# Kernel tuning notes

Hardware: AMD Instinct MI355X
Metric: run time of the kernel (lower is better)

The kernel has to match this reference:

```python
import jax, jax.numpy as jnp
import numpy as np

B, S, T, V, D = 256, 256, 256, 512, 512


def _gru_cell(x, h, Wih, Whh, bih, bhh):
    # torch GRU semantics: gates ordered [r, z, n]
    gi = x @ Wih.T + bih            # [B, 3D]
    gh = h @ Whh.T + bhh            # [B, 3D]
    gi_r, gi_z, gi_n = jnp.split(gi, 3, axis=-1)
    gh_r, gh_z, gh_n = jnp.split(gh, 3, axis=-1)
    r = jax.nn.sigmoid(gi_r + gh_r)
    z = jax.nn.sigmoid(gi_z + gh_z)
    n = jnp.tanh(gi_n + r * gh_n)
    return (1.0 - z) * n + z * h


def setup_inputs() -> dict:
    key = jax.random.key(0)
    ks = jax.random.split(key, 14)
    s = 0.05
    inp = {
        "src": jax.random.randint(ks[0], (B, S), 0, V),
        "trg": jax.random.randint(ks[1], (B, T), 0, V),
        "src_mask": jnp.ones((B, S), dtype=bool),
        "trg_mask": jnp.ones((B, T), dtype=bool),
        "enc_emb": jax.random.normal(ks[2], (V, D), jnp.float32) * s,
        "enc_Wih": jax.random.normal(ks[3], (3 * D, D), jnp.float32) * s,
        "enc_Whh": jax.random.normal(ks[4], (3 * D, D), jnp.float32) * s,
        "enc_bih": jnp.zeros((3 * D,), jnp.float32),
        "enc_bhh": jnp.zeros((3 * D,), jnp.float32),
        "dec_emb": jax.random.normal(ks[5], (V, D), jnp.float32) * s,
        "dec_Wih": jax.random.normal(ks[6], (3 * D, D), jnp.float32) * s,
        "dec_Whh": jax.random.normal(ks[7], (3 * D, D), jnp.float32) * s,
        "dec_bih": jnp.zeros((3 * D,), jnp.float32),
        "dec_bhh": jnp.zeros((3 * D,), jnp.float32),
        "out_W": jax.random.normal(ks[8], (V, D), jnp.float32) * s,
        "out_b": jnp.zeros((V,), jnp.float32),
    }
    return inp


def reference(src, trg, src_mask, trg_mask,
              enc_emb, enc_Wih, enc_Whh, enc_bih, enc_bhh,
              dec_emb, dec_Wih, dec_Whh, dec_bih, dec_bhh,
              out_W, out_b):
    b = src.shape[0]
    d = enc_Whh.shape[1]

    # ---- encoder: embed (eval: no dropout) + GRU over src ----
    enc_x = enc_emb[src]                       # [B, S, D]
    h0 = jnp.zeros((b, d), enc_emb.dtype)

    def enc_step(h, x):
        return _gru_cell(x, h, enc_Wih, enc_Whh, enc_bih, enc_bhh), None

    h_enc, _ = jax.lax.scan(enc_step, h0, jnp.swapaxes(enc_x, 0, 1))

    # ---- decoder: relu(embed) + GRU step + linear per timestep ----
    dec_x = jax.nn.relu(dec_emb[trg])          # [B, T, D]

    def dec_step(h, x):
        h = _gru_cell(x, h, dec_Wih, dec_Whh, dec_bih, dec_bhh)
        logits = h @ out_W.T + out_b           # [B, V]
        return h, logits

    _, logits = jax.lax.scan(dec_step, h_enc, jnp.swapaxes(dec_x, 0, 1))
    logits = jnp.swapaxes(logits, 0, 1)        # [B, T, V]
    return jax.nn.log_softmax(logits, axis=-1)
```

## Files before the change

### kernel.cpp

```cpp
#include <hip/hip_runtime.h>
#include <cstdint>
#include <cstddef>

namespace {
constexpr int Dh = 512;
constexpr int G3 = 1536;
constexpr int NB = 256;
constexpr int SL = 256;
constexpr int TL = 256;
constexpr int NV = 512;
}

typedef __attribute__((ext_vector_type(8))) short bf16x8;
typedef __attribute__((ext_vector_type(4))) float f32x4;

__device__ __forceinline__ unsigned short f2bf(float f) {
  unsigned int u = __float_as_uint(f);
  u = (u + 0x7FFFu + ((u >> 16) & 1u)) >> 16;
  return (unsigned short)u;
}
__device__ __forceinline__ float bf2f(unsigned short s) {
  return __uint_as_float(((unsigned int)s) << 16);
}

__global__ __launch_bounds__(256) void cvt_bf16(const float* __restrict__ in,
                                                unsigned short* __restrict__ out,
                                                int n4, int relu) {
  int i = blockIdx.x * 256 + threadIdx.x;
  if (i >= n4) return;
  float4 v = ((const float4*)in)[i];
  if (relu) {
    v.x = fmaxf(v.x, 0.f); v.y = fmaxf(v.y, 0.f);
    v.z = fmaxf(v.z, 0.f); v.w = fmaxf(v.w, 0.f);
  }
  ushort4 o;
  o.x = f2bf(v.x); o.y = f2bf(v.y); o.z = f2bf(v.z); o.w = f2bf(v.w);
  ((ushort4*)out)[i] = o;
}

template <int AMODE, bool OUTBF16>
__global__ __launch_bounds__(256) void gemm_bf16(
    const unsigned short* __restrict__ Abase, const int* __restrict__ idx,
    const unsigned short* __restrict__ W, const float* __restrict__ bias,
    void* __restrict__ Cout, int N) {
  __shared__ unsigned short lds_a[8 * 128 * 8];
  __shared__ unsigned short lds_b[8 * 128 * 8];
  const int t = threadIdx.x;
  const int n0 = blockIdx.x * 128;
  const int m0 = blockIdx.y * 128;
  const int w = t >> 6, l = t & 63;
  const int mq = (w & 1) * 64, nq = (w >> 1) * 64;
  const int l15 = l & 15, lh = l >> 4;

  const int sm = t & 127;
  const int sk = (t >> 7) * 4;
  const unsigned short* arow;
  if (AMODE == 0) {
    arow = Abase + (size_t)idx[m0 + sm] * Dh;
  } else {
    int row = m0 + sm;
    arow = Abase + ((size_t)(row & 255) * NB + (row >> 8)) * Dh;
  }
  const unsigned short* brow = W + (size_t)(n0 + sm) * Dh;

  f32x4 acc[4][4];
#pragma unroll
  for (int i = 0; i < 4; ++i)
#pragma unroll
    for (int j = 0; j < 4; ++j) acc[i][j] = (f32x4)0.f;

  for (int k0 = 0; k0 < Dh; k0 += 64) {
    __syncthreads();
#pragma unroll
    for (int i = 0; i < 4; ++i) {
      int kc = sk + i;
      *(uint4*)&lds_a[(kc * 128 + sm) * 8] = *(const uint4*)(arow + k0 + kc * 8);
      *(uint4*)&lds_b[(kc * 128 + sm) * 8] = *(const uint4*)(brow + k0 + kc * 8);
    }
    __syncthreads();
#pragma unroll
    for (int q = 0; q < 2; ++q) {
      bf16x8 af[4], bfr[4];
#pragma unroll
      for (int i = 0; i < 4; ++i)
        af[i] = *(const bf16x8*)&lds_a[((q * 4 + lh) * 128 + mq + i * 16 + l15) * 8];
#pragma unroll
      for (int j = 0; j < 4; ++j)
        bfr[j] = *(const bf16x8*)&lds_b[((q * 4 + lh) * 128 + nq + j * 16 + l15) * 8];
#pragma unroll
      for (int i = 0; i < 4; ++i)
#pragma unroll
        for (int j = 0; j < 4; ++j)
          acc[i][j] = __builtin_amdgcn_mfma_f32_16x16x32_bf16(af[i], bfr[j], acc[i][j], 0, 0, 0);
    }
  }

#pragma unroll
  for (int j = 0; j < 4; ++j) {
    const int col = n0 + nq + j * 16 + l15;
    const float bv = bias[col];
#pragma unroll
    for (int i = 0; i < 4; ++i) {
#pragma unroll
      for (int r = 0; r < 4; ++r) {
        const size_t row = (size_t)m0 + mq + i * 16 + lh * 4 + r;
        const float v = acc[i][j][r] + bv;
        if (OUTBF16)
          ((unsigned short*)Cout)[row * N + col] = f2bf(v);
        else
          ((float*)Cout)[row * N + col] = v;
      }
    }
  }
}

__global__ __launch_bounds__(256) void gru_step(
    const float* __restrict__ h_in, const unsigned short* __restrict__ hb_in,
    float* __restrict__ h_out, unsigned short* __restrict__ hb_out,
    const unsigned short* __restrict__ W,
    const unsigned short* __restrict__ gi,
    const float* __restrict__ bhh, int tstep, int seq) {
  __shared__ unsigned short lds_w[64 * 48 * 8];
  __shared__ float lds_red[4 * 6 * 256];
  const int t = threadIdx.x;
  const int d0 = blockIdx.x * 16;
  const int b0 = blockIdx.y * 32;
  const int w = t >> 6, l = t & 63;
  const int l15 = l & 15, lh = l >> 4;

#pragma unroll
  for (int i = 0; i < 12; ++i) {
    int id = i * 256 + t;
    int kc = id & 63, c = id >> 6;
    int gate = c >> 4, dl = c & 15;
    const unsigned short* src = W + (size_t)(gate * Dh + d0 + dl) * Dh + kc * 8;
    *(uint4*)&lds_w[(kc * 48 + c) * 8] = *(const uint4*)src;
  }

  f32x4 acc[2][3];
#pragma unroll
  for (int mi = 0; mi < 2; ++mi)
#pragma unroll
    for (int nj = 0; nj < 3; ++nj) acc[mi][nj] = (f32x4)0.f;

  __syncthreads();

#pragma unroll
  for (int q = 0; q < 4; ++q) {
    const int kc32 = w * 4 + q;
    bf16x8 a[2], bfr[3];
#pragma unroll
    for (int mi = 0; mi < 2; ++mi)
      a[mi] = *(const bf16x8*)(hb_in + (size_t)(b0 + mi * 16 + l15) * Dh + kc32 * 32 + lh * 8);
#pragma unroll
    for (int nj = 0; nj < 3; ++nj)
      bfr[nj] = *(const bf16x8*)&lds_w[((kc32 * 4 + lh) * 48 + nj * 16 + l15) * 8];
#pragma unroll
    for (int mi = 0; mi < 2; ++mi)
#pragma unroll
      for (int nj = 0; nj < 3; ++nj)
        acc[mi][nj] = __builtin_amdgcn_mfma_f32_16x16x32_bf16(a[mi], bfr[nj], acc[mi][nj], 0, 0, 0);
  }

#pragma unroll
  for (int mi = 0; mi < 2; ++mi)
#pragma unroll
    for (int nj = 0; nj < 3; ++nj)
#pragma unroll
      for (int r = 0; r < 4; ++r)
        lds_red[(w * 6 + mi * 3 + nj) * 256 + (lh * 4 + r) * 16 + l15] = acc[mi][nj][r];
  __syncthreads();

  const int bl = t >> 3;
  const int dl = (t & 7) * 2;
  const int mi = bl >> 4, row = bl & 15;
  float gh[3][2];
#pragma unroll
  for (int g = 0; g < 3; ++g)
#pragma unroll
    for (int dd = 0; dd < 2; ++dd) {
      float s = 0.f;
#pragma unroll
      for (int ww = 0; ww < 4; ++ww)
        s += lds_red[(ww * 6 + mi * 3 + g) * 256 + row * 16 + dl + dd];
      gh[g][dd] = s;
    }

  const int b = b0 + bl;
  const int d = d0 + dl;
  const unsigned short* gr = gi + ((size_t)b * seq + tstep) * G3;
  ushort2 ur = *(const ushort2*)&gr[d];
  ushort2 uz = *(const ushort2*)&gr[Dh + d];
  ushort2 un = *(const ushort2*)&gr[2 * Dh + d];
  float2 hp = *(const float2*)&h_in[(size_t)b * Dh + d];
  float2 br = *(const float2*)&bhh[d];
  float2 bz = *(const float2*)&bhh[Dh + d];
  float2 bn = *(const float2*)&bhh[2 * Dh + d];
  const float gir[2] = {bf2f(ur.x), bf2f(ur.y)};
  const float giz[2] = {bf2f(uz.x), bf2f(uz.y)};
  const float gin[2] = {bf2f(un.x), bf2f(un.y)};
  const float brv[2] = {br.x, br.y}, bzv[2] = {bz.x, bz.y}, bnv[2] = {bn.x, bn.y};
  const float hpv[2] = {hp.x, hp.y};
  float o[2];
#pragma unroll
  for (int dd = 0; dd < 2; ++dd) {
    float rr = 1.f / (1.f + expf(-(gir[dd] + gh[0][dd] + brv[dd])));
    float zz = 1.f / (1.f + expf(-(giz[dd] + gh[1][dd] + bzv[dd])));
    float nn = tanhf(gin[dd] + rr * (gh[2][dd] + bnv[dd]));
    o[dd] = (1.f - zz) * nn + zz * hpv[dd];
  }
  float2 ov; ov.x = o[0]; ov.y = o[1];
  *(float2*)&h_out[(size_t)b * Dh + d] = ov;
  ushort2 ob; ob.x = f2bf(o[0]); ob.y = f2bf(o[1]);
  *(ushort2*)&hb_out[(size_t)b * Dh + d] = ob;
}

__global__ __launch_bounds__(256) void logsoftmax512(float* __restrict__ x) {
  const int row = blockIdx.x * 4 + (threadIdx.x >> 6);
  const int lane = threadIdx.x & 63;
  float* p = x + (size_t)row * NV + lane * 8;
  float4 v0 = *(const float4*)p;
  float4 v1 = *(const float4*)(p + 4);
  float m = fmaxf(fmaxf(fmaxf(v0.x, v0.y), fmaxf(v0.z, v0.w)),
                  fmaxf(fmaxf(v1.x, v1.y), fmaxf(v1.z, v1.w)));
#pragma unroll
  for (int o = 1; o < 64; o <<= 1) m = fmaxf(m, __shfl_xor(m, o, 64));
  float s = expf(v0.x - m) + expf(v0.y - m) + expf(v0.z - m) + expf(v0.w - m) +
            expf(v1.x - m) + expf(v1.y - m) + expf(v1.z - m) + expf(v1.w - m);
#pragma unroll
  for (int o = 1; o < 64; o <<= 1) s += __shfl_xor(s, o, 64);
  const float ls = m + logf(s);
  v0.x -= ls; v0.y -= ls; v0.z -= ls; v0.w -= ls;
  v1.x -= ls; v1.y -= ls; v1.z -= ls; v1.w -= ls;
  *(float4*)p = v0;
  *(float4*)(p + 4) = v1;
}

extern "C" void kernel_launch(void* const* d_in, const int* in_sizes, int n_in,
                              void* d_out, int out_size, void* d_ws, size_t ws_size,
                              hipStream_t stream) {
  (void)in_sizes; (void)n_in; (void)out_size; (void)ws_size;
  const int* src = (const int*)d_in[0];
  const int* trg = (const int*)d_in[1];
  const float* enc_emb = (const float*)d_in[4];
  const float* enc_Wih = (const float*)d_in[5];
  const float* enc_Whh = (const float*)d_in[6];
  const float* enc_bih = (const float*)d_in[7];
  const float* enc_bhh = (const float*)d_in[8];
  const float* dec_emb = (const float*)d_in[9];
  const float* dec_Wih = (const float*)d_in[10];
  const float* dec_Whh = (const float*)d_in[11];
  const float* dec_bih = (const float*)d_in[12];
  const float* dec_bhh = (const float*)d_in[13];
  const float* out_W = (const float*)d_in[14];
  const float* out_b = (const float*)d_in[15];

  char* ws = (char*)d_ws;
  size_t off = 0;
  auto alloc = [&](size_t bytes) -> char* {
    char* p = ws + off;
    off += (bytes + 255) & ~(size_t)255;
    return p;
  };
  typedef unsigned short u16;
  u16* gi = (u16*)alloc((size_t)NB * SL * G3 * 2);
  u16* hb_all = (u16*)alloc((size_t)TL * NB * Dh * 2);
  float* h_a = (float*)alloc((size_t)NB * Dh * 4);
  float* h_b = (float*)alloc((size_t)NB * Dh * 4);
  u16* hb_a = (u16*)alloc((size_t)NB * Dh * 2);
  u16* hb_b = (u16*)alloc((size_t)NB * Dh * 2);
  u16* embB_e = (u16*)alloc((size_t)NV * Dh * 2);
  u16* embB_d = (u16*)alloc((size_t)NV * Dh * 2);
  u16* WihB_e = (u16*)alloc((size_t)G3 * Dh * 2);
  u16* WhhB_e = (u16*)alloc((size_t)G3 * Dh * 2);
  u16* WihB_d = (u16*)alloc((size_t)G3 * Dh * 2);
  u16* WhhB_d = (u16*)alloc((size_t)G3 * Dh * 2);
  u16* outWB = (u16*)alloc((size_t)NV * Dh * 2);

  cvt_bf16<<<(NV * Dh / 4 + 255) / 256, 256, 0, stream>>>(enc_emb, embB_e, NV * Dh / 4, 0);
  cvt_bf16<<<(NV * Dh / 4 + 255) / 256, 256, 0, stream>>>(dec_emb, embB_d, NV * Dh / 4, 1);
  cvt_bf16<<<(G3 * Dh / 4 + 255) / 256, 256, 0, stream>>>(enc_Wih, WihB_e, G3 * Dh / 4, 0);
  cvt_bf16<<<(G3 * Dh / 4 + 255) / 256, 256, 0, stream>>>(enc_Whh, WhhB_e, G3 * Dh / 4, 0);
  cvt_bf16<<<(G3 * Dh / 4 + 255) / 256, 256, 0, stream>>>(dec_Wih, WihB_d, G3 * Dh / 4, 0);
  cvt_bf16<<<(G3 * Dh / 4 + 255) / 256, 256, 0, stream>>>(dec_Whh, WhhB_d, G3 * Dh / 4, 0);
  cvt_bf16<<<(NV * Dh / 4 + 255) / 256, 256, 0, stream>>>(out_W, outWB, NV * Dh / 4, 0);
  hipMemsetAsync(h_a, 0, (size_t)NB * Dh * 4, stream);
  hipMemsetAsync(hb_a, 0, (size_t)NB * Dh * 2, stream);

  dim3 ggi(G3 / 128, NB * SL / 128);
  gemm_bf16<0, true><<<ggi, 256, 0, stream>>>(embB_e, src, WihB_e, enc_bih, gi, G3);

  dim3 gstep(Dh / 16, NB / 32);
  for (int t = 0; t < SL; ++t) {
    const float* hi = (t & 1) ? h_b : h_a;
    float* ho = (t & 1) ? h_a : h_b;
    const u16* hbi = (t & 1) ? hb_b : hb_a;
    u16* hbo = (t & 1) ? hb_a : hb_b;
    gru_step<<<gstep, 256, 0, stream>>>(hi, hbi, ho, hbo, WhhB_e, gi, enc_bhh, t, SL);
  }

  gemm_bf16<0, true><<<ggi, 256, 0, stream>>>(embB_d, trg, WihB_d, dec_bih, gi, G3);

  for (int t = 0; t < TL; ++t) {
    const float* hi = (t & 1) ? h_b : h_a;
    float* ho = (t & 1) ? h_a : h_b;
    const u16* hbi = (t == 0) ? hb_a : (hb_all + (size_t)(t - 1) * NB * Dh);
    u16* hbo = hb_all + (size_t)t * NB * Dh;
    gru_step<<<gstep, 256, 0, stream>>>(hi, hbi, ho, hbo, WhhB_d, gi, dec_bhh, t, TL);
  }

  dim3 glg(NV / 128, NB * TL / 128);
  gemm_bf16<1, false><<<glg, 256, 0, stream>>>(hb_all, nullptr, outWB, out_b, d_out, NV);
  logsoftmax512<<<NB * TL / 4, 256, 0, stream>>>((float*)d_out);
}
```

Baseline: 3.787 ms.

## Fuse GRU timestep launches into a persistent cooperative kernel with grid barriers

Replaces the 256 per-timestep launches in both the encoder and the decoder with one cooperative persistent kernel per phase. Steps are separated by an atomic-counter grid barrier. The Whh tile fragments stay in registers and the fp32 hidden state stays in registers across steps, so the weight reload from memory and the per-step launch overhead go away. In exchange, each step now pays a global spin barrier. The barrier also depends on cross-block memory visibility through a single-thread release/acquire, which could expose stale cached reads.

```diff
diff --git a/kernel.cpp b/kernel.cpp
--- a/kernel.cpp
+++ b/kernel.cpp
@@ -114,17 +114,23 @@
   }
 }
 
-__global__ __launch_bounds__(256) void gru_step(
-    const float* __restrict__ h_in, const unsigned short* __restrict__ hb_in,
-    float* __restrict__ h_out, unsigned short* __restrict__ hb_out,
+__global__ __launch_bounds__(256) void gru_phase(
     const unsigned short* __restrict__ W,
     const unsigned short* __restrict__ gi,
-    const float* __restrict__ bhh, int tstep, int seq) {
+    const float* __restrict__ bhh,
+    unsigned short* __restrict__ hb0,
+    unsigned short* __restrict__ hb1,
+    const float* __restrict__ h0_in,
+    float* __restrict__ h_final,
+    unsigned short* __restrict__ hb_all,
+    unsigned int* __restrict__ counter,
+    int nsteps) {
   __shared__ unsigned short lds_w[64 * 48 * 8];
   __shared__ float lds_red[4 * 6 * 256];
   const int t = threadIdx.x;
-  const int d0 = blockIdx.x * 16;
-  const int b0 = blockIdx.y * 32;
+  const int bid = blockIdx.x;
+  const int d0 = (bid & 31) * 16;
+  const int b0 = (bid >> 5) * 32;
   const int w = t >> 6, l = t & 63;
   const int l15 = l & 15, lh = l >> 4;
 
@@ -132,87 +138,125 @@
   for (int i = 0; i < 12; ++i) {
     int id = i * 256 + t;
     int kc = id & 63, c = id >> 6;
-    int gate = c >> 4, dl = c & 15;
-    const unsigned short* src = W + (size_t)(gate * Dh + d0 + dl) * Dh + kc * 8;
+    int gate = c >> 4, dl_ = c & 15;
+    const unsigned short* src = W + (size_t)(gate * Dh + d0 + dl_) * Dh + kc * 8;
     *(uint4*)&lds_w[(kc * 48 + c) * 8] = *(const uint4*)src;
   }
-
-  f32x4 acc[2][3];
-#pragma unroll
-  for (int mi = 0; mi < 2; ++mi)
-#pragma unroll
-    for (int nj = 0; nj < 3; ++nj) acc[mi][nj] = (f32x4)0.f;
-
   __syncthreads();
 
+  bf16x8 bfr[4][3];
 #pragma unroll
   for (int q = 0; q < 4; ++q) {
     const int kc32 = w * 4 + q;
-    bf16x8 a[2], bfr[3];
-#pragma unroll
-    for (int mi = 0; mi < 2; ++mi)
-      a[mi] = *(const bf16x8*)(hb_in + (size_t)(b0 + mi * 16 + l15) * Dh + kc32 * 32 + lh * 8);
 #pragma unroll
     for (int nj = 0; nj < 3; ++nj)
-      bfr[nj] = *(const bf16x8*)&lds_w[((kc32 * 4 + lh) * 48 + nj * 16 + l15) * 8];
-#pragma unroll
-    for (int mi = 0; mi < 2; ++mi)
-#pragma unroll
-      for (int nj = 0; nj < 3; ++nj)
-        acc[mi][nj] = __builtin_amdgcn_mfma_f32_16x16x32_bf16(a[mi], bfr[nj], acc[mi][nj], 0, 0, 0);
-  }
-
-#pragma unroll
-  for (int mi = 0; mi < 2; ++mi)
-#pragma unroll
-    for (int nj = 0; nj < 3; ++nj)
-#pragma unroll
-      for (int r = 0; r < 4; ++r)
-        lds_red[(w * 6 + mi * 3 + nj) * 256 + (lh * 4 + r) * 16 + l15] = acc[mi][nj][r];
-  __syncthreads();
+      bfr[q][nj] = *(const bf16x8*)&lds_w[((kc32 * 4 + lh) * 48 + nj * 16 + l15) * 8];
+  }
 
   const int bl = t >> 3;
   const int dl = (t & 7) * 2;
-  const int mi = bl >> 4, row = bl & 15;
-  float gh[3][2];
-#pragma unroll
-  for (int g = 0; g < 3; ++g)
-#pragma unroll
-    for (int dd = 0; dd < 2; ++dd) {
-      float s = 0.f;
-#pragma unroll
-      for (int ww = 0; ww < 4; ++ww)
-        s += lds_red[(ww * 6 + mi * 3 + g) * 256 + row * 16 + dl + dd];
-      gh[g][dd] = s;
-    }
-
+  const int mi_e = bl >> 4, row_e = bl & 15;
   const int b = b0 + bl;
   const int d = d0 + dl;
-  const unsigned short* gr = gi + ((size_t)b * seq + tstep) * G3;
-  ushort2 ur = *(const ushort2*)&gr[d];
-  ushort2 uz = *(const ushort2*)&gr[Dh + d];
-  ushort2 un = *(const ushort2*)&gr[2 * Dh + d];
-  float2 hp = *(const float2*)&h_in[(size_t)b * Dh + d];
-  float2 br = *(const float2*)&bhh[d];
-  float2 bz = *(const float2*)&bhh[Dh + d];
-  float2 bn = *(const float2*)&bhh[2 * Dh + d];
-  const float gir[2] = {bf2f(ur.x), bf2f(ur.y)};
-  const float giz[2] = {bf2f(uz.x), bf2f(uz.y)};
-  const float gin[2] = {bf2f(un.x), bf2f(un.y)};
-  const float brv[2] = {br.x, br.y}, bzv[2] = {bz.x, bz.y}, bnv[2] = {bn.x, bn.y};
-  const float hpv[2] = {hp.x, hp.y};
-  float o[2];
-#pragma unroll
-  for (int dd = 0; dd < 2; ++dd) {
-    float rr = 1.f / (1.f + expf(-(gir[dd] + gh[0][dd] + brv[dd])));
-    float zz = 1.f / (1.f + expf(-(giz[dd] + gh[1][dd] + bzv[dd])));
-    float nn = tanhf(gin[dd] + rr * (gh[2][dd] + bnv[dd]));
-    o[dd] = (1.f - zz) * nn + zz * hpv[dd];
-  }
-  float2 ov; ov.x = o[0]; ov.y = o[1];
-  *(float2*)&h_out[(size_t)b * Dh + d] = ov;
-  ushort2 ob; ob.x = f2bf(o[0]); ob.y = f2bf(o[1]);
-  *(ushort2*)&hb_out[(size_t)b * Dh + d] = ob;
+  const float2 br = *(const float2*)&bhh[d];
+  const float2 bz = *(const float2*)&bhh[Dh + d];
+  const float2 bn = *(const float2*)&bhh[2 * Dh + d];
+  float2 hp;
+  if (h0_in) hp = *(const float2*)&h0_in[(size_t)b * Dh + d];
+  else { hp.x = 0.f; hp.y = 0.f; }
+
+  size_t aoff[2];
+#pragma unroll
+  for (int mi = 0; mi < 2; ++mi)
+    aoff[mi] = (size_t)(b0 + mi * 16 + l15) * Dh + w * 128 + lh * 8;
+
+  const unsigned short* gbase = gi + (size_t)b * 256 * G3;
+  ushort2 ur = *(const ushort2*)&gbase[d];
+  ushort2 uz = *(const ushort2*)&gbase[Dh + d];
+  ushort2 un = *(const ushort2*)&gbase[2 * Dh + d];
+
+  for (int s = 0; s < nsteps; ++s) {
+    const unsigned short* hin = (s & 1) ? hb1 : hb0;
+    unsigned short* hout = (s & 1) ? hb0 : hb1;
+
+    f32x4 acc[2][3];
+#pragma unroll
+    for (int mi = 0; mi < 2; ++mi)
+#pragma unroll
+      for (int nj = 0; nj < 3; ++nj) acc[mi][nj] = (f32x4)0.f;
+
+#pragma unroll
+    for (int q = 0; q < 4; ++q) {
+      bf16x8 a[2];
+#pragma unroll
+      for (int mi = 0; mi < 2; ++mi)
+        a[mi] = *(const bf16x8*)(hin + aoff[mi] + q * 32);
+#pragma unroll
+      for (int mi = 0; mi < 2; ++mi)
+#pragma unroll
+        for (int nj = 0; nj < 3; ++nj)
+          acc[mi][nj] = __builtin_amdgcn_mfma_f32_16x16x32_bf16(a[mi], bfr[q][nj], acc[mi][nj], 0, 0, 0);
+    }
+
+    __syncthreads();
+#pragma unroll
+    for (int mi = 0; mi < 2; ++mi)
+#pragma unroll
+      for (int nj = 0; nj < 3; ++nj)
+#pragma unroll
+        for (int r = 0; r < 4; ++r)
+          lds_red[(w * 6 + mi * 3 + nj) * 256 + (lh * 4 + r) * 16 + l15] = acc[mi][nj][r];
+    __syncthreads();
+
+    float gh[3][2];
+#pragma unroll
+    for (int g = 0; g < 3; ++g)
+#pragma unroll
+      for (int dd = 0; dd < 2; ++dd) {
+        float ssum = 0.f;
+#pragma unroll
+        for (int ww = 0; ww < 4; ++ww)
+          ssum += lds_red[(ww * 6 + mi_e * 3 + g) * 256 + row_e * 16 + dl + dd];
+        gh[g][dd] = ssum;
+      }
+
+    const float gir[2] = {bf2f(ur.x), bf2f(ur.y)};
+    const float giz[2] = {bf2f(uz.x), bf2f(uz.y)};
+    const float gin[2] = {bf2f(un.x), bf2f(un.y)};
+    const float brv[2] = {br.x, br.y}, bzv[2] = {bz.x, bz.y}, bnv[2] = {bn.x, bn.y};
+    float hpv[2] = {hp.x, hp.y};
+    float o[2];
+#pragma unroll
+    for (int dd = 0; dd < 2; ++dd) {
+      float rr = 1.f / (1.f + expf(-(gir[dd] + gh[0][dd] + brv[dd])));
+      float zz = 1.f / (1.f + expf(-(giz[dd] + gh[1][dd] + bzv[dd])));
+      float nn = tanhf(gin[dd] + rr * (gh[2][dd] + bnv[dd]));
+      o[dd] = (1.f - zz) * nn + zz * hpv[dd];
+    }
+    hp.x = o[0]; hp.y = o[1];
+
+    ushort2 ob; ob.x = f2bf(o[0]); ob.y = f2bf(o[1]);
+    *(ushort2*)&hout[(size_t)b * Dh + d] = ob;
+    if (hb_all) *(ushort2*)&hb_all[((size_t)s * NB + b) * Dh + d] = ob;
+    if (h_final && s == nsteps - 1) *(float2*)&h_final[(size_t)b * Dh + d] = hp;
+
+    if (s + 1 < nsteps) {
+      const unsigned short* gr = gbase + (size_t)(s + 1) * G3;
+      ur = *(const ushort2*)&gr[d];
+      uz = *(const ushort2*)&gr[Dh + d];
+      un = *(const ushort2*)&gr[2 * Dh + d];
+    }
+
+    if (s + 1 < nsteps) {
+      __syncthreads();
+      if (t == 0) {
+        __hip_atomic_fetch_add(counter, 1u, __ATOMIC_RELEASE, __HIP_MEMORY_SCOPE_AGENT);
+        const unsigned int tgt = 256u * (unsigned)(s + 1);
+        while (__hip_atomic_load(counter, __ATOMIC_ACQUIRE, __HIP_MEMORY_SCOPE_AGENT) < tgt) {}
+      }
+      __syncthreads();
+    }
+  }
 }
 
 __global__ __launch_bounds__(256) void logsoftmax512(float* __restrict__ x) {
@@ -265,10 +309,9 @@
   typedef unsigned short u16;
   u16* gi = (u16*)alloc((size_t)NB * SL * G3 * 2);
   u16* hb_all = (u16*)alloc((size_t)TL * NB * Dh * 2);
-  float* h_a = (float*)alloc((size_t)NB * Dh * 4);
-  float* h_b = (float*)alloc((size_t)NB * Dh * 4);
-  u16* hb_a = (u16*)alloc((size_t)NB * Dh * 2);
-  u16* hb_b = (u16*)alloc((size_t)NB * Dh * 2);
+  u16* hb0 = (u16*)alloc((size_t)NB * Dh * 2);
+  u16* hb1 = (u16*)alloc((size_t)NB * Dh * 2);
+  float* h_enc = (float*)alloc((size_t)NB * Dh * 4);
   u16* embB_e = (u16*)alloc((size_t)NV * Dh * 2);
   u16* embB_d = (u16*)alloc((size_t)NV * Dh * 2);
   u16* WihB_e = (u16*)alloc((size_t)G3 * Dh * 2);
@@ -276,6 +319,7 @@
   u16* WihB_d = (u16*)alloc((size_t)G3 * Dh * 2);
   u16* WhhB_d = (u16*)alloc((size_t)G3 * Dh * 2);
   u16* outWB = (u16*)alloc((size_t)NV * Dh * 2);
+  unsigned int* ctr = (unsigned int*)alloc(256);
 
   cvt_bf16<<<(NV * Dh / 4 + 255) / 256, 256, 0, stream>>>(enc_emb, embB_e, NV * Dh / 4, 0);
   cvt_bf16<<<(NV * Dh / 4 + 255) / 256, 256, 0, stream>>>(dec_emb, embB_d, NV * Dh / 4, 1);
@@ -284,29 +328,31 @@
   cvt_bf16<<<(G3 * Dh / 4 + 255) / 256, 256, 0, stream>>>(dec_Wih, WihB_d, G3 * Dh / 4, 0);
   cvt_bf16<<<(G3 * Dh / 4 + 255) / 256, 256, 0, stream>>>(dec_Whh, WhhB_d, G3 * Dh / 4, 0);
   cvt_bf16<<<(NV * Dh / 4 + 255) / 256, 256, 0, stream>>>(out_W, outWB, NV * Dh / 4, 0);
-  hipMemsetAsync(h_a, 0, (size_t)NB * Dh * 4, stream);
-  hipMemsetAsync(hb_a, 0, (size_t)NB * Dh * 2, stream);
+  hipMemsetAsync(hb0, 0, (size_t)NB * Dh * 2, stream);
+  hipMemsetAsync(ctr, 0, 8, stream);
 
   dim3 ggi(G3 / 128, NB * SL / 128);
   gemm_bf16<0, true><<<ggi, 256, 0, stream>>>(embB_e, src, WihB_e, enc_bih, gi, G3);
 
-  dim3 gstep(Dh / 16, NB / 32);
-  for (int t = 0; t < SL; ++t) {
-    const float* hi = (t & 1) ? h_b : h_a;
-    float* ho = (t & 1) ? h_a : h_b;
-    const u16* hbi = (t & 1) ? hb_b : hb_a;
-    u16* hbo = (t & 1) ? hb_a : hb_b;
-    gru_step<<<gstep, 256, 0, stream>>>(hi, hbi, ho, hbo, WhhB_e, gi, enc_bhh, t, SL);
+  int ns = 256;
+  {
+    const u16* Wp = WhhB_e; const u16* gip = gi; const float* bp = enc_bhh;
+    u16* p0 = hb0; u16* p1 = hb1;
+    const float* h0n = nullptr; float* hf = h_enc; u16* hba = nullptr;
+    unsigned int* c0 = ctr;
+    void* args[] = {&Wp, &gip, &bp, &p0, &p1, &h0n, &hf, &hba, &c0, &ns};
+    hipLaunchCooperativeKernel((void*)gru_phase, dim3(256), dim3(256), args, 0, stream);
   }
 
   gemm_bf16<0, true><<<ggi, 256, 0, stream>>>(embB_d, trg, WihB_d, dec_bih, gi, G3);
 
-  for (int t = 0; t < TL; ++t) {
-    const float* hi = (t & 1) ? h_b : h_a;
-    float* ho = (t & 1) ? h_a : h_b;
-    const u16* hbi = (t == 0) ? hb_a : (hb_all + (size_t)(t - 1) * NB * Dh);
-    u16* hbo = hb_all + (size_t)t * NB * Dh;
-    gru_step<<<gstep, 256, 0, stream>>>(hi, hbi, ho, hbo, WhhB_d, gi, dec_bhh, t, TL);
+  {
+    const u16* Wp = WhhB_d; const u16* gip = gi; const float* bp = dec_bhh;
+    u16* p0 = hb0; u16* p1 = hb1;
+    const float* h0n = h_enc; float* hf = nullptr; u16* hba = hb_all;
+    unsigned int* c1 = ctr + 1;
+    void* args[] = {&Wp, &gip, &bp, &p0, &p1, &h0n, &hf, &hba, &c1, &ns};
+    hipLaunchCooperativeKernel((void*)gru_phase, dim3(256), dim3(256), args, 0, stream);
   }
 
   dim3 glg(NV / 128, NB * TL / 128);
```

Result: slower. 12.23 ms (+223.0%).
